# Optimization experiments

Measured on AMD Instinct MI355X. Metric: run time of the kernel, lower is better.

Reference implementation:

```python
import jax, jax.numpy as jnp
import numpy as np

N = 100000      # points
M = 12500       # cluster centers
E0 = 1600000    # point-level edges
E1 = 400000     # cluster-level edges
F_IN = 4        # raw point feature dim (e.g. intensity + extras)
D = 64          # hidden feature width
N_CLASSES = 8


def setup_inputs() -> dict:
    key = jax.random.key(0)
    ks = jax.random.split(key, 20)
    s = 0.05
    d = {}
    d["features"] = jax.random.normal(ks[0], (N, F_IN), jnp.float32)
    d["points"] = jax.random.normal(ks[1], (N, 3), jnp.float32)
    d["cluster_centers"] = jax.random.normal(ks[2], (M, 3), jnp.float32)
    d["l0_edges"] = jax.random.randint(ks[3], (E0, 2), 0, N)
    d["l1_edges"] = jax.random.randint(ks[4], (E1, 2), 0, M)
    d["labels"] = jax.random.randint(ks[5], (N,), 0, M)
    # Feature_extract MLP
    d["W_fe"] = s * jax.random.normal(ks[6], (F_IN + 3, D), jnp.float32)
    d["b_fe"] = jnp.zeros((D,), jnp.float32)
    # 4 Mini_GNN layers (layer2, layer2_1, layer6, layer6_1), stacked
    d["mini_We"] = s * jax.random.normal(ks[7], (4, D + 3, D), jnp.float32)
    d["mini_be"] = jnp.zeros((4, D), jnp.float32)
    d["mini_Wu"] = s * jax.random.normal(ks[8], (4, D, D), jnp.float32)
    d["mini_bu"] = jnp.zeros((4, D), jnp.float32)
    # Mini_to_Large
    d["W_m1"] = s * jax.random.normal(ks[9], (D + 3, D), jnp.float32)
    d["b_m1"] = jnp.zeros((D,), jnp.float32)
    d["W_m2"] = s * jax.random.normal(ks[10], (D, D), jnp.float32)
    d["b_m2"] = jnp.zeros((D,), jnp.float32)
    # 2 GNN layers on cluster graph (layer4, layer4_1), stacked
    d["gnn_We"] = s * jax.random.normal(ks[11], (2, D + 3, D), jnp.float32)
    d["gnn_be"] = jnp.zeros((2, D), jnp.float32)
    d["gnn_Wu"] = s * jax.random.normal(ks[12], (2, D, D), jnp.float32)
    d["gnn_bu"] = jnp.zeros((2, D), jnp.float32)
    # Large_to_Mini
    d["W_l"] = s * jax.random.normal(ks[13], (D + 3, D), jnp.float32)
    d["b_l"] = jnp.zeros((D,), jnp.float32)
    # Classifier
    d["W_c"] = s * jax.random.normal(ks[14], (D, N_CLASSES), jnp.float32)
    d["b_c"] = jnp.zeros((N_CLASSES,), jnp.float32)
    return d


def _gnn_layer(feat, pos, edges, We, be, Wu, bu, n_nodes):
    """PointGNN-style layer: gather -> edge MLP -> scatter max -> update MLP -> residual."""
    src, dst = edges[:, 0], edges[:, 1]
    e_in = jnp.concatenate([pos[src] - pos[dst], feat[src]], axis=-1)  # [E, 3+D]
    h = jax.nn.relu(e_in @ We + be)                                     # [E, D]
    agg = jax.ops.segment_max(h, dst, num_segments=n_nodes)            # [n, D]
    agg = jnp.where(jnp.isneginf(agg), 0.0, agg)  # nodes with no in-edges -> 0
    return jax.nn.relu(agg @ Wu + bu) + feat


def reference(features, points, cluster_centers, l0_edges, l1_edges, labels,
              W_fe, b_fe, mini_We, mini_be, mini_Wu, mini_bu,
              W_m1, b_m1, W_m2, b_m2, gnn_We, gnn_be, gnn_Wu, gnn_bu,
              W_l, b_l, W_c, b_c):
    rel = points - cluster_centers[labels]  # [N, 3] point pos relative to its cluster
    # layer1: Feature_extract
    f1 = jax.nn.relu(jnp.concatenate([features, rel], -1) @ W_fe + b_fe)
    # layer2 / layer2_1: Mini_GNN (scatter max) on point graph
    f2 = _gnn_layer(f1, points, l0_edges, mini_We[0], mini_be[0], mini_Wu[0], mini_bu[0], N)
    f2_1 = _gnn_layer(f2, points, l0_edges, mini_We[1], mini_be[1], mini_Wu[1], mini_bu[1], N)
    # layer3: Mini_to_Large (scatter sum by labels)
    h = jax.nn.relu(jnp.concatenate([f2_1, rel], -1) @ W_m1 + b_m1)
    c = jax.ops.segment_sum(h, labels, num_segments=M)  # [M, D]
    f3 = jax.nn.relu(c @ W_m2 + b_m2)
    # layer4 / layer4_1: GNN (scatter max) on cluster graph
    f4 = _gnn_layer(f3, cluster_centers, l1_edges, gnn_We[0], gnn_be[0], gnn_Wu[0], gnn_bu[0], M)
    f4_1 = _gnn_layer(f4, cluster_centers, l1_edges, gnn_We[1], gnn_be[1], gnn_Wu[1], gnn_bu[1], M)
    # layer5: Large_to_Mini (gather by labels)
    f5 = jax.nn.relu(jnp.concatenate([f4_1[labels], rel], -1) @ W_l + b_l)
    # layer6 / layer6_1 with residual skips per call()
    f6 = _gnn_layer(f5, points, l0_edges, mini_We[2], mini_be[2], mini_Wu[2], mini_bu[2], N)
    f6 = f6 + f2_1
    f6_1 = _gnn_layer(f6, points, l0_edges, mini_We[3], mini_be[3], mini_Wu[3], mini_bu[3], N)
    final = f6_1 + f2
    return final @ W_c + b_c  # [N, N_CLASSES] per-point logits
```

## Files before the change

### kernel.cpp

```cpp
#include <hip/hip_runtime.h>


#define N_PTS   100000
#define M_CL    12500
#define E0_N    1600000
#define E1_N    400000

#define NB      256
#define NCOPY   32
#define RANGE0  391
#define RANGE1  49
#define NCH0    782
#define NCH1    196
#define NCHL    49
#define CAP0    7168
#define CAP1    2048
#define CAPL    768

#define LSTR    72

typedef unsigned short ushortT;
typedef short  short8 __attribute__((ext_vector_type(8)));
typedef short  s4v    __attribute__((ext_vector_type(4)));
typedef float  v4f    __attribute__((ext_vector_type(4)));
typedef _Float16 h2   __attribute__((ext_vector_type(2)));
typedef unsigned u4v  __attribute__((ext_vector_type(4)));

__device__ inline ushortT f2bf(float x){
  union{float f; unsigned u;} v; v.f = x;
  unsigned r = v.u + 0x7fffu + ((v.u >> 16) & 1u);
  return (ushortT)(r >> 16);
}
__device__ inline float bf2f(ushortT h){
  union{unsigned u; float f;} v; v.u = ((unsigned)h) << 16;
  return v.f;
}
__device__ inline ushortT f2h(float x){
  union{_Float16 h; ushortT u;} v; v.h = (_Float16)x;
  return v.u;
}
__device__ inline float h2f(ushortT u){
  union{ushortT u; _Float16 h;} v; v.u = u;
  return (float)v.h;
}
__device__ inline h2 pkmax(h2 a, h2 b){ return __builtin_elementwise_max(a, b); }
__device__ inline h2 u2h(unsigned u){ union{unsigned u; h2 h;} v{u}; return v.h; }

struct WSrc { const float* p[22]; };


template<int RANGE, bool LAB>
__device__ void sort_chunk(const int* __restrict__ edges, int E, int c,
                           unsigned* __restrict__ slab, int* __restrict__ offC,
                           int* __restrict__ btot,
                           unsigned* slds, int* hist, int* pfx){
  int tid = threadIdx.x;
  int base = c*2048;
  int cnt = E - base; if (cnt > 2048) cnt = 2048;
  hist[tid] = 0;
  __syncthreads();
  int bk[8]; unsigned pk[8];
  #pragma unroll
  for (int r=0;r<8;++r){
    int e = base + r*256 + tid;
    bk[r] = -1; pk[r] = 0;
    if (e < E){
      int s, d;
      if (LAB){ s = e; d = edges[e]; }
      else    { int2 ed = ((const int2*)edges)[e]; s = ed.x; d = ed.y; }
      int b = d / RANGE;
      bk[r] = b;
      pk[r] = ((unsigned)s << 11) | (unsigned)(d - b*RANGE);
      atomicAdd(&hist[b], 1);
    }
  }
  __syncthreads();
  int own = hist[tid];
  pfx[tid] = own;
  __syncthreads();
  for (int st=1; st<256; st<<=1){
    int x = (tid >= st) ? pfx[tid-st] : 0;
    __syncthreads();
    pfx[tid] += x;
    __syncthreads();
  }
  int excl = pfx[tid] - own;
  offC[(size_t)c*257 + tid] = excl;
  if (tid == 0) offC[(size_t)c*257 + 256] = cnt;
  if (own) atomicAdd(&btot[(c & (NCOPY-1))*NB + tid], own);
  hist[tid] = excl;
  __syncthreads();
  #pragma unroll
  for (int r=0;r<8;++r){
    if (bk[r] >= 0){
      int pos = atomicAdd(&hist[bk[r]], 1);
      slds[pos] = pk[r];
    }
  }
  __syncthreads();
  unsigned* sg = slab + (size_t)c*2048;
  for (int i=tid; i<cnt; i+=256) sg[i] = slds[i];
}


template<int RANGE, int NCHUNK, int K>
__device__ void csr_build_seg(const unsigned* __restrict__ slab, const int* __restrict__ offC,
                              const int* __restrict__ btot,
                              int n, int* __restrict__ offs, int* __restrict__ csr,
                              int b, unsigned* stage, int* hist, int* part,
                              ushortT* mstA, ushortT* mlenA, ushortT* sbA){
  constexpr int CPT = (NCHUNK + 255) / 256;
  int tid = threadIdx.x;
  int dlo = b*RANGE;
  int range = n - dlo; if (range > RANGE) range = RANGE; if (range < 0) range = 0;
  int ownT = 0;
  #pragma unroll
  for (int k=0;k<NCOPY;++k) ownT += btot[k*NB + tid];
  part[tid] = ownT;
  __syncthreads();
  for (int st=1; st<256; st<<=1){
    int x = (tid >= st) ? part[tid-st] : 0;
    __syncthreads();
    part[tid] += x;
    __syncthreads();
  }
  int totB = part[b];
  int total = part[NB-1];
  if (b == NB-1 && tid == 0) offs[n] = total;
  __syncthreads();
  int mst[CPT], mlen[CPT];
  int csum = 0;
  #pragma unroll
  for (int k=0;k<CPT;++k){
    int c = tid + k*256;
    int l = 0, s0 = 0;
    if (c < NCHUNK){
      s0 = offC[(size_t)c*257 + b];
      l  = offC[(size_t)c*257 + b + 1] - s0;
    }
    mst[k] = s0; mlen[k] = l; csum += l;
  }
  part[tid] = csum;
  __syncthreads();
  int own2 = csum;
  for (int st=1; st<256; st<<=1){
    int x = (tid >= st) ? part[tid-st] : 0;
    __syncthreads();
    part[tid] += x;
    __syncthreads();
  }
  int cnt = part[NB-1];
  int gb = totB - cnt;
  int sb = part[tid] - own2;
  #pragma unroll
  for (int k=0;k<CPT;++k){
    int c = tid + k*256;
    if (c < NCHUNK){
      mstA[c] = (ushortT)mst[k];
      mlenA[c] = (ushortT)mlen[k];
      sbA[c] = (ushortT)sb;
      sb += mlen[k];
    }
  }
  __syncthreads();
  int wv = tid >> 6, l = tid & 63;
  for (int cb = wv*32; cb < NCHUNK; cb += 128){
    int c = cb + (l >> 1);
    if (c < NCHUNK){
      int len = mlenA[c];
      int half = l & 1;
      if (half*4 < len){
        const unsigned* sg = slab + (size_t)c*2048 + mstA[c];
        int sbc = sbA[c];
        for (int j = half*4; j < len; j += 8){
          unsigned v[4];
          __builtin_memcpy(v, sg + j, 16);
          #pragma unroll
          for (int q=0;q<4;++q) if (j+q < len) stage[sbc+j+q] = v[q];
        }
      }
    }
  }
  __syncthreads();
  for (int t=tid; t<RANGE; t+=256) hist[t] = 0;
  __syncthreads();
  for (int j=tid; j<cnt; j+=256) atomicAdd(&hist[stage[j] & 2047u], 1);
  __syncthreads();
  int s = 0; int loc[K];
  #pragma unroll
  for (int kk=0; kk<K; ++kk){
    int idx = tid*K + kk;
    int v = (idx < RANGE) ? hist[idx] : 0;
    loc[kk] = s; s += v;
  }
  part[tid] = s; __syncthreads();
  int own3 = s;
  for (int st=1; st<256; st<<=1){
    int x = (tid >= st) ? part[tid-st] : 0;
    __syncthreads();
    part[tid] += x;
    __syncthreads();
  }
  int ebase = part[tid] - own3;
  __syncthreads();
  #pragma unroll
  for (int kk=0; kk<K; ++kk){
    int idx = tid*K + kk;
    if (idx < RANGE){
      int ex = ebase + loc[kk];
      if (idx < range) offs[dlo+idx] = gb + ex;
      hist[idx] = ex;
    }
  }
  __syncthreads();
  for (int j=tid; j<cnt; j+=256){
    unsigned p = stage[j];
    int pos = atomicAdd(&hist[p & 2047u], 1);
    csr[gb + pos] = (int)(p >> 11);
  }
}

__global__ __launch_bounds__(256) void k_build_all(
    const unsigned* s0, const int* oc0, const int* bt0, int* offs0, int* csr0,
    const unsigned* s1, const int* oc1, const int* bt1, int* offs1, int* csr1,
    const unsigned* sL, const int* ocL, const int* btL, int* offsL, int* csrL){
  __shared__ unsigned stage[CAP0];
  __shared__ int hist[RANGE0];
  __shared__ int part[256];
  __shared__ ushortT mstA[NCH0];
  __shared__ ushortT mlenA[NCH0];
  __shared__ ushortT sbA[NCH0];
  int b = blockIdx.x;
  if (b < 256)      csr_build_seg<RANGE0,NCH0,2>(s0, oc0, bt0, N_PTS, offs0, csr0, b, stage, hist, part, mstA, mlenA, sbA);
  else if (b < 512) csr_build_seg<RANGE1,NCH1,1>(s1, oc1, bt1, M_CL, offs1, csr1, b-256, stage, hist, part, mstA, mlenA, sbA);
  else              csr_build_seg<RANGE1,NCHL,1>(sL, ocL, btL, M_CL, offsL, csrL, b-512, stage, hist, part, mstA, mlenA, sbA);
}


__global__ __launch_bounds__(256) void k_bin_f1g(
    WSrc s, ushortT* __restrict__ wt, ushortT* __restrict__ wtc, float* __restrict__ wpp,
    const int* __restrict__ l0e, const int* __restrict__ l1e, const int* __restrict__ labels,
    int* bt0, int* bt1, int* btL,
    unsigned* sl0, unsigned* sl1, unsigned* slL,
    int* oc0, int* oc1, int* ocL,
    const float* __restrict__ features, const float* __restrict__ points,
    const float* __restrict__ centers,
    const float* __restrict__ W, const float* __restrict__ bfe,
    const float* __restrict__ bias2, const float* __restrict__ We,
    float* __restrict__ rel, ushortT* __restrict__ f1b,
    ushortT* __restrict__ gout, int n, int ntiles, int nf1blk)
{
  __shared__ char smem[10240];
  int b = blockIdx.x;
  if (b < 17){
    int slot = b;
    if (slot < 15){
      const float* src = s.p[slot];
      ushortT* dst = wt + slot*4096;
      for (int e=threadIdx.x; e<4096; e+=256){
        int nn = e>>6, p = e&63;
        int kk = (p&3)*16 + (p>>2);
        dst[e] = f2bf(src[kk*64+nn]);
      }
    } else if (slot == 15){
      const float* src = s.p[15];
      for (int e=threadIdx.x; e<1024; e+=256){
        int nn = e>>6, p = e&63;
        int kk = (p&3)*16 + (p>>2);
        wtc[e] = (nn<8) ? f2bf(src[kk*8+nn]) : (ushortT)0;
      }
    } else {
      for (int e=threadIdx.x; e<6*192; e+=256){
        int i = e/192, rem = e - i*192, r = rem>>6, p = rem&63;
        wpp[e] = s.p[16+i][r*64 + ((p&3)*16 + (p>>2))];
      }
    }
    return;
  }
  b -= 17;
  if (b < 1027){
    unsigned* slds = (unsigned*)smem;
    int* hist = (int*)(smem + 8192);
    int* pfx  = (int*)(smem + 9216);
    if (b < 782)      sort_chunk<RANGE0,false>(l0e, E0_N, b,     sl0, oc0, bt0, slds, hist, pfx);
    else if (b < 978) sort_chunk<RANGE1,false>(l1e, E1_N, b-782, sl1, oc1, bt1, slds, hist, pfx);
    else              sort_chunk<RANGE1,true >(labels, N_PTS, b-978, slL, ocL, btL, slds, hist, pfx);
    return;
  }
  ushortT* lds = (ushortT*)smem;
  int bb = b - 1027;
  int tid = threadIdx.x;
  int lane = tid & 63, wslot = tid >> 6;
  int quad = lane >> 4, l15 = lane & 15;
  int permL = (lane & 15)*4 + (lane >> 4);
  int r3 = lane/3, c3 = lane - r3*3;
  int gw = (bb*256 + tid) >> 6;
  int nw = (nf1blk*256) >> 6;
  float Wf0=W[0*64+lane], Wf1=W[1*64+lane], Wf2=W[2*64+lane], Wf3=W[3*64+lane];
  float wr0=W[4*64+lane], wr1=W[5*64+lane], wr2=W[6*64+lane];
  float bias=bfe[lane];
  const float* Wk = We + 192;
  auto ldf = [&](int nn, int pbase)->short8{
    short8 r;
    #pragma unroll
    for (int e=0;e<8;++e){
      int p = pbase + e;
      int kk = (p&3)*16 + (p>>2);
      r[e] = (short)f2bf(Wk[kk*64 + nn]);
    }
    return r;
  };
  short8 s0_0 = ldf(l15, quad*8),      s0_1 = ldf(l15, 32+quad*8);
  short8 s1_0 = ldf(16+l15, quad*8),   s1_1 = ldf(16+l15, 32+quad*8);
  short8 s2_0 = ldf(32+l15, quad*8),   s2_1 = ldf(32+l15, 32+quad*8);
  short8 s3_0 = ldf(48+l15, quad*8),   s3_1 = ldf(48+l15, 32+quad*8);
  float eb0 = bias2[l15], eb1 = bias2[16+l15], eb2 = bias2[32+l15], eb3 = bias2[48+l15];
  float e0c0=We[0*64+l15], e0c1=We[0*64+16+l15], e0c2=We[0*64+32+l15], e0c3=We[0*64+48+l15];
  float e1c0=We[1*64+l15], e1c1=We[1*64+16+l15], e1c2=We[1*64+32+l15], e1c3=We[1*64+48+l15];
  float e2c0=We[2*64+l15], e2c1=We[2*64+16+l15], e2c2=We[2*64+32+l15], e2c3=We[2*64+48+l15];

  for (int t=gw; t<ntiles; t+=nw){
    int i0 = t*16;
    int lab16 = labels[min(i0 + (lane & 15), n-1)];
    float fv  = features[(size_t)min(i0 + (lane>>2), n-1)*4 + (lane & 3)];
    int lb = __shfl(lab16, (r3 < 16) ? r3 : 0, 64);
    float pv = 0.f, relv = 0.f;
    if (lane < 48){
      int rowp = i0 + r3;
      int rc = (rowp < n) ? rowp : (n-1);
      pv = points[(size_t)rc*3 + c3];
      float cv = centers[(size_t)lb*3 + c3];
      relv = pv - cv;
      if (rowp < n) rel[(size_t)rowp*3 + c3] = relv;
    }
    #pragma unroll
    for (int r=0;r<16;++r){
      float rx = __shfl(relv, 3*r+0, 64);
      float ry = __shfl(relv, 3*r+1, 64);
      float rz = __shfl(relv, 3*r+2, 64);
      float f0 = __shfl(fv, 4*r+0, 64);
      float f1 = __shfl(fv, 4*r+1, 64);
      float f2 = __shfl(fv, 4*r+2, 64);
      float f3 = __shfl(fv, 4*r+3, 64);
      float acc = bias + wr0*rx + wr1*ry + wr2*rz;
      acc += f0*Wf0 + f1*Wf1;
      acc += f2*Wf2 + f3*Wf3;
      acc = fmaxf(acc, 0.f);
      ushortT ab = f2bf(acc);
      int row = i0 + r;
      if (row < n) f1b[(size_t)row*64 + permL] = ab;
      lds[wslot*(16*LSTR) + r*LSTR + permL] = ab;
    }
    __builtin_amdgcn_wave_barrier();
    const ushortT* lp = lds + wslot*(16*LSTR) + l15*LSTR + quad*8;
    short8 sa0 = *(const short8*)(lp);
    short8 sa1 = *(const short8*)(lp + 32);
    __builtin_amdgcn_wave_barrier();
    v4f ec0 = {0.f,0.f,0.f,0.f}, ec1 = ec0, ec2 = ec0, ec3 = ec0;
    ec0 = __builtin_amdgcn_mfma_f32_16x16x32_bf16(sa0, s0_0, ec0, 0,0,0);
    ec1 = __builtin_amdgcn_mfma_f32_16x16x32_bf16(sa0, s1_0, ec1, 0,0,0);
    ec2 = __builtin_amdgcn_mfma_f32_16x16x32_bf16(sa0, s2_0, ec2, 0,0,0);
    ec3 = __builtin_amdgcn_mfma_f32_16x16x32_bf16(sa0, s3_0, ec3, 0,0,0);
    ec0 = __builtin_amdgcn_mfma_f32_16x16x32_bf16(sa1, s0_1, ec0, 0,0,0);
    ec1 = __builtin_amdgcn_mfma_f32_16x16x32_bf16(sa1, s1_1, ec1, 0,0,0);
    ec2 = __builtin_amdgcn_mfma_f32_16x16x32_bf16(sa1, s2_1, ec2, 0,0,0);
    ec3 = __builtin_amdgcn_mfma_f32_16x16x32_bf16(sa1, s3_1, ec3, 0,0,0);
    #pragma unroll
    for (int r=0;r<4;++r){
      int row = i0 + quad*4 + r;
      if (row < n){
        int rr4 = quad*4 + r;
        float vx = __shfl(pv, 3*rr4+0, 64);
        float vy = __shfl(pv, 3*rr4+1, 64);
        float vz = __shfl(pv, 3*rr4+2, 64);
        float g0 = ec0[r] + eb0 + vx*e0c0 + vy*e1c0 + vz*e2c0;
        float g1 = ec1[r] + eb1 + vx*e0c1 + vy*e1c1 + vz*e2c1;
        float g2 = ec2[r] + eb2 + vx*e0c2 + vy*e1c2 + vz*e2c2;
        float g3 = ec3[r] + eb3 + vx*e0c3 + vy*e1c3 + vz*e2c3;
        s4v o; o.x=(short)f2h(g0); o.y=(short)f2h(g1); o.z=(short)f2h(g2); o.w=(short)f2h(g3);
        *(s4v*)(gout + (size_t)row*64 + l15*4) = o;
      }
    }
  }
}


template<bool RELU, int NRES, bool USEREL, bool GATHER, bool OUT16, bool F16O, int EMODE, bool ERELU>
__global__ __launch_bounds__(256) void k_gemm(
    const ushortT* __restrict__ A, const ushortT* __restrict__ Wt,
    const float* __restrict__ bias, const float* __restrict__ Wr,
    const float* __restrict__ rel, const int* __restrict__ gidx,
    const ushortT* __restrict__ r1, const ushortT* __restrict__ r2,
    ushortT* __restrict__ out16,
    const ushortT* __restrict__ Wt2, const float* __restrict__ bias2,
    const float* __restrict__ Wr2, const float* __restrict__ vec2,
    void* __restrict__ eout,
    int n, int ntiles)
{
  constexpr int LDSZ = (EMODE>0) ? 4*16*LSTR : 4;
  __shared__ ushortT lds[LDSZ];
  int tid = threadIdx.x;
  int lane = tid & 63, wslot = tid >> 6;
  int quad = lane >> 4, l15 = lane & 15;
  int r3 = lane/3, c3 = lane - r3*3;
  int gw = (blockIdx.x*256 + tid) >> 6;
  int nw = (gridDim.x*256) >> 6;

  short8 bfr0_0 = *(const short8*)(Wt + ( 0 + l15)*64 +  0 + quad*8);
  short8 bfr0_1 = *(const short8*)(Wt + ( 0 + l15)*64 + 32 + quad*8);
  short8 bfr1_0 = *(const short8*)(Wt + (16 + l15)*64 +  0 + quad*8);
  short8 bfr1_1 = *(const short8*)(Wt + (16 + l15)*64 + 32 + quad*8);
  short8 bfr2_0 = *(const short8*)(Wt + (32 + l15)*64 +  0 + quad*8);
  short8 bfr2_1 = *(const short8*)(Wt + (32 + l15)*64 + 32 + quad*8);
  short8 bfr3_0 = *(const short8*)(Wt + (48 + l15)*64 +  0 + quad*8);
  short8 bfr3_1 = *(const short8*)(Wt + (48 + l15)*64 + 32 + quad*8);
  float bs0 = bias[ 0 + l15], bs1 = bias[16 + l15];
  float bs2 = bias[32 + l15], bs3 = bias[48 + l15];
  float w0c0=0,w0c1=0,w0c2=0,w0c3=0, w1c0=0,w1c1=0,w1c2=0,w1c3=0, w2c0=0,w2c1=0,w2c2=0,w2c3=0;
  if (USEREL){
    w0c0=Wr[0*64+l15]; w0c1=Wr[0*64+16+l15]; w0c2=Wr[0*64+32+l15]; w0c3=Wr[0*64+48+l15];
    w1c0=Wr[1*64+l15]; w1c1=Wr[1*64+16+l15]; w1c2=Wr[1*64+32+l15]; w1c3=Wr[1*64+48+l15];
    w2c0=Wr[2*64+l15]; w2c1=Wr[2*64+16+l15]; w2c2=Wr[2*64+32+l15]; w2c3=Wr[2*64+48+l15];
  }

  short8 s0_0{}, s0_1{}, s1_0{}, s1_1{}, s2_0{}, s2_1{}, s3_0{}, s3_1{};
  float eb0=0, eb1=0, eb2=0, eb3=0;
  float e0c0=0,e0c1=0,e0c2=0,e0c3=0, e1c0=0,e1c1=0,e1c2=0,e1c3=0, e2c0=0,e2c1=0,e2c2=0,e2c3=0;
  float ebias_c = 0.f;
  if (EMODE == 1){
    s0_0 = *(const short8*)(Wt2 + ( 0 + l15)*64 +  0 + quad*8);
    s0_1 = *(const short8*)(Wt2 + ( 0 + l15)*64 + 32 + quad*8);
    s1_0 = *(const short8*)(Wt2 + (16 + l15)*64 +  0 + quad*8);
    s1_1 = *(const short8*)(Wt2 + (16 + l15)*64 + 32 + quad*8);
    s2_0 = *(const short8*)(Wt2 + (32 + l15)*64 +  0 + quad*8);
    s2_1 = *(const short8*)(Wt2 + (32 + l15)*64 + 32 + quad*8);
    s3_0 = *(const short8*)(Wt2 + (48 + l15)*64 +  0 + quad*8);
    s3_1 = *(const short8*)(Wt2 + (48 + l15)*64 + 32 + quad*8);
    eb0 = bias2[l15]; eb1 = bias2[16+l15]; eb2 = bias2[32+l15]; eb3 = bias2[48+l15];
    e0c0=Wr2[0*64+l15]; e0c1=Wr2[0*64+16+l15]; e0c2=Wr2[0*64+32+l15]; e0c3=Wr2[0*64+48+l15];
    e1c0=Wr2[1*64+l15]; e1c1=Wr2[1*64+16+l15]; e1c2=Wr2[1*64+32+l15]; e1c3=Wr2[1*64+48+l15];
    e2c0=Wr2[2*64+l15]; e2c1=Wr2[2*64+16+l15]; e2c2=Wr2[2*64+32+l15]; e2c3=Wr2[2*64+48+l15];
  } else if (EMODE == 2){
    s0_0 = *(const short8*)(Wt2 + l15*64 +  0 + quad*8);
    s0_1 = *(const short8*)(Wt2 + l15*64 + 32 + quad*8);
    ebias_c = (l15 < 8) ? bias2[l15] : 0.f;
  }

  for (int t=gw; t<ntiles; t+=nw){
    int i0 = t*16;
    int rowA = i0 + l15; if (rowA >= n) rowA = n-1;
    if (GATHER) rowA = gidx[rowA];
    const ushortT* ap = A + (size_t)rowA*64 + quad*8;
    short8 a0 = *(const short8*)(ap);
    short8 a1 = *(const short8*)(ap + 32);
    float relL = 0.f;
    if (USEREL && lane < 48){
      int rc = i0 + r3; if (rc >= n) rc = n-1;
      relL = rel[(size_t)rc*3 + c3];
    }
    v4f ac0 = {0.f,0.f,0.f,0.f}, ac1 = ac0, ac2 = ac0, ac3 = ac0;
    ac0 = __builtin_amdgcn_mfma_f32_16x16x32_bf16(a0, bfr0_0, ac0, 0,0,0);
    ac1 = __builtin_amdgcn_mfma_f32_16x16x32_bf16(a0, bfr1_0, ac1, 0,0,0);
    ac2 = __builtin_amdgcn_mfma_f32_16x16x32_bf16(a0, bfr2_0, ac2, 0,0,0);
    ac3 = __builtin_amdgcn_mfma_f32_16x16x32_bf16(a0, bfr3_0, ac3, 0,0,0);
    ac0 = __builtin_amdgcn_mfma_f32_16x16x32_bf16(a1, bfr0_1, ac0, 0,0,0);
    ac1 = __builtin_amdgcn_mfma_f32_16x16x32_bf16(a1, bfr1_1, ac1, 0,0,0);
    ac2 = __builtin_amdgcn_mfma_f32_16x16x32_bf16(a1, bfr2_1, ac2, 0,0,0);
    ac3 = __builtin_amdgcn_mfma_f32_16x16x32_bf16(a1, bfr3_1, ac3, 0,0,0);

    #pragma unroll
    for (int r=0;r<4;++r){
      int row = i0 + quad*4 + r;
      bool rowok = (row < n);
      float v0 = ac0[r] + bs0, v1 = ac1[r] + bs1, v2 = ac2[r] + bs2, v3 = ac3[r] + bs3;
      if (USEREL){
        int rr4 = quad*4 + r;
        float rx = __shfl(relL, 3*rr4+0, 64);
        float ry = __shfl(relL, 3*rr4+1, 64);
        float rz = __shfl(relL, 3*rr4+2, 64);
        v0 += rx*w0c0 + ry*w1c0 + rz*w2c0;
        v1 += rx*w0c1 + ry*w1c1 + rz*w2c1;
        v2 += rx*w0c2 + ry*w1c2 + rz*w2c2;
        v3 += rx*w0c3 + ry*w1c3 + rz*w2c3;
      }
      if (RELU){ v0=fmaxf(v0,0.f); v1=fmaxf(v1,0.f); v2=fmaxf(v2,0.f); v3=fmaxf(v3,0.f); }
      size_t pb = (size_t)row*64 + l15*4;
      if (rowok){
        if (NRES>=1){
          s4v rv = *(const s4v*)(r1 + pb);
          v0 += bf2f((ushortT)rv.x); v1 += bf2f((ushortT)rv.y);
          v2 += bf2f((ushortT)rv.z); v3 += bf2f((ushortT)rv.w);
        }
        if (NRES>=2){
          s4v rv = *(const s4v*)(r2 + pb);
          v0 += bf2f((ushortT)rv.x); v1 += bf2f((ushortT)rv.y);
          v2 += bf2f((ushortT)rv.z); v3 += bf2f((ushortT)rv.w);
        }
        if (OUT16){
          s4v o;
          if (F16O){ o.x=(short)f2h(v0); o.y=(short)f2h(v1); o.z=(short)f2h(v2); o.w=(short)f2h(v3); }
          else     { o.x=(short)f2bf(v0); o.y=(short)f2bf(v1); o.z=(short)f2bf(v2); o.w=(short)f2bf(v3); }
          *(s4v*)(out16 + pb) = o;
        }
      }
      if (EMODE > 0){
        int lb = wslot*(16*LSTR) + (quad*4+r)*LSTR + l15*4;
        s4v o; o.x=(short)f2bf(v0); o.y=(short)f2bf(v1); o.z=(short)f2bf(v2); o.w=(short)f2bf(v3);
        *(s4v*)(lds + lb) = o;
      }
    }

    if (EMODE > 0){
      __builtin_amdgcn_wave_barrier();
      const ushortT* lp = lds + wslot*(16*LSTR) + l15*LSTR + quad*8;
      short8 sa0 = *(const short8*)(lp);
      short8 sa1 = *(const short8*)(lp + 32);
      __builtin_amdgcn_wave_barrier();
      if (EMODE == 1){
        float posv = 0.f;
        if (lane < 48){
          int rc = i0 + r3; if (rc >= n) rc = n-1;
          posv = vec2[(size_t)rc*3 + c3];
        }
        v4f ec0 = {0.f,0.f,0.f,0.f}, ec1 = ec0, ec2 = ec0, ec3 = ec0;
        ec0 = __builtin_amdgcn_mfma_f32_16x16x32_bf16(sa0, s0_0, ec0, 0,0,0);
        ec1 = __builtin_amdgcn_mfma_f32_16x16x32_bf16(sa0, s1_0, ec1, 0,0,0);
        ec2 = __builtin_amdgcn_mfma_f32_16x16x32_bf16(sa0, s2_0, ec2, 0,0,0);
        ec3 = __builtin_amdgcn_mfma_f32_16x16x32_bf16(sa0, s3_0, ec3, 0,0,0);
        ec0 = __builtin_amdgcn_mfma_f32_16x16x32_bf16(sa1, s0_1, ec0, 0,0,0);
        ec1 = __builtin_amdgcn_mfma_f32_16x16x32_bf16(sa1, s1_1, ec1, 0,0,0);
        ec2 = __builtin_amdgcn_mfma_f32_16x16x32_bf16(sa1, s2_1, ec2, 0,0,0);
        ec3 = __builtin_amdgcn_mfma_f32_16x16x32_bf16(sa1, s3_1, ec3, 0,0,0);
        ushortT* eo = (ushortT*)eout;
        #pragma unroll
        for (int r=0;r<4;++r){
          int row = i0 + quad*4 + r;
          if (row < n){
            int rr4 = quad*4 + r;
            float vx = __shfl(posv, 3*rr4+0, 64);
            float vy = __shfl(posv, 3*rr4+1, 64);
            float vz = __shfl(posv, 3*rr4+2, 64);
            float g0 = ec0[r] + eb0 + vx*e0c0 + vy*e1c0 + vz*e2c0;
            float g1 = ec1[r] + eb1 + vx*e0c1 + vy*e1c1 + vz*e2c1;
            float g2 = ec2[r] + eb2 + vx*e0c2 + vy*e1c2 + vz*e2c2;
            float g3 = ec3[r] + eb3 + vx*e0c3 + vy*e1c3 + vz*e2c3;
            if (ERELU){ g0=fmaxf(g0,0.f); g1=fmaxf(g1,0.f); g2=fmaxf(g2,0.f); g3=fmaxf(g3,0.f); }
            s4v o; o.x=(short)f2h(g0); o.y=(short)f2h(g1); o.z=(short)f2h(g2); o.w=(short)f2h(g3);
            *(s4v*)(eo + (size_t)row*64 + l15*4) = o;
          }
        }
      } else {
        v4f ec = {0.f,0.f,0.f,0.f};
        ec = __builtin_amdgcn_mfma_f32_16x16x32_bf16(sa0, s0_0, ec, 0,0,0);
        ec = __builtin_amdgcn_mfma_f32_16x16x32_bf16(sa1, s0_1, ec, 0,0,0);
        if (l15 < 8){
          float* eo = (float*)eout;
          #pragma unroll
          for (int r=0;r<4;++r){
            int row = i0 + quad*4 + r;
            if (row < n) eo[(size_t)row*8 + l15] = ec[r] + ebias_c;
          }
        }
      }
    }
  }
}


__global__ __launch_bounds__(256) void k_edge_agg(const int* __restrict__ offs, const int* __restrict__ csr,
                                                  const float* __restrict__ pos, const ushortT* __restrict__ g,
                                                  const float* __restrict__ Wp, ushortT* __restrict__ agg, int n){
  int lane = threadIdx.x & 63;
  int grp = lane >> 3, d8 = lane & 7;
  int gbase = lane & 56;
  int gw = (blockIdx.x*256 + threadIdx.x) >> 6;
  int nw = (gridDim.x*256) >> 6;
  const u4v* g4 = (const u4v*)g;
  float2 w0[4], w1[4], w2[4];
  #pragma unroll
  for (int q=0;q<4;++q){
    w0[q] = *(const float2*)(Wp + 0*64 + d8*8 + 2*q);
    w1[q] = *(const float2*)(Wp + 1*64 + d8*8 + 2*q);
    w2[q] = *(const float2*)(Wp + 2*64 + d8*8 + 2*q);
  }
  const h2 NEGBIG = {(_Float16)-60000.f, (_Float16)-60000.f};
  int n8 = (n+7) >> 3;
  for (int ii=gw; ii<n8; ii+=nw){
    int i0 = ii*8;
    int ig = i0 + grp; bool ok = ig < n; if (!ok) ig = n-1;
    int b = offs[ig], e = offs[ig+1];
    int cnt = e - b, c1 = cnt - 1;
    int mx = cnt;
    mx = max(mx, __shfl_xor(mx, 8, 64));
    mx = max(mx, __shfl_xor(mx, 16, 64));
    mx = max(mx, __shfl_xor(mx, 32, 64));
    h2 m0=NEGBIG, m1=NEGBIG, m2=NEGBIG, m3=NEGBIG;
    for (int J=0; J<mx; J+=8){
      if (J < cnt){
        int sv = csr[b + min(J + d8, c1)];
        #pragma unroll
        for (int jj=0; jj<8; ++jj){
          int s = __shfl(sv, gbase + jj, 64);
          u4v u = g4[(size_t)s*8 + d8];
          m0 = pkmax(m0, u2h(u.x));
          m1 = pkmax(m1, u2h(u.y));
          m2 = pkmax(m2, u2h(u.z));
          m3 = pkmax(m3, u2h(u.w));
        }
      }
    }
    float px = pos[ig*3+0], py = pos[ig*3+1], pz = pos[ig*3+2];
    u4v outv;
    {
      float sA = w0[0].x*px + w1[0].x*py + w2[0].x*pz;
      float sB = w0[0].y*px + w1[0].y*py + w2[0].y*pz;
      outv.x = (unsigned)f2bf(fmaxf((float)m0.x - sA, 0.f)) |
               ((unsigned)f2bf(fmaxf((float)m0.y - sB, 0.f)) << 16);
    }
    {
      float sA = w0[1].x*px + w1[1].x*py + w2[1].x*pz;
      float sB = w0[1].y*px + w1[1].y*py + w2[1].y*pz;
      outv.y = (unsigned)f2bf(fmaxf((float)m1.x - sA, 0.f)) |
               ((unsigned)f2bf(fmaxf((float)m1.y - sB, 0.f)) << 16);
    }
    {
      float sA = w0[2].x*px + w1[2].x*py + w2[2].x*pz;
      float sB = w0[2].y*px + w1[2].y*py + w2[2].y*pz;
      outv.z = (unsigned)f2bf(fmaxf((float)m2.x - sA, 0.f)) |
               ((unsigned)f2bf(fmaxf((float)m2.y - sB, 0.f)) << 16);
    }
    {
      float sA = w0[3].x*px + w1[3].x*py + w2[3].x*pz;
      float sB = w0[3].y*px + w1[3].y*py + w2[3].y*pz;
      outv.w = (unsigned)f2bf(fmaxf((float)m3.x - sA, 0.f)) |
               ((unsigned)f2bf(fmaxf((float)m3.y - sB, 0.f)) << 16);
    }
    if (ok) ((u4v*)agg)[(size_t)ig*8 + d8] = outv;
  }
}


__global__ __launch_bounds__(256) void k_seg_gather(const int* __restrict__ offs, const int* __restrict__ csr,
                                                    const ushortT* __restrict__ h, ushortT* __restrict__ c, int m){
  int lane = threadIdx.x & 63;
  int wv = (blockIdx.x*256 + threadIdx.x) >> 6;
  if (wv >= m) return;
  int b = offs[wv], e = offs[wv+1];
  float acc = 0.f;
  for (int k=b; k<e; ++k){
    int i = csr[k];
    acc += h2f(h[(size_t)i*64+lane]);
  }
  c[(size_t)wv*64+lane] = f2bf(acc);
}


extern "C" void kernel_launch(void* const* d_in, const int* in_sizes, int n_in,
                              void* d_out, int out_size, void* d_ws, size_t ws_size,
                              hipStream_t stream){
  const float* features = (const float*)d_in[0];
  const float* points   = (const float*)d_in[1];
  const float* centers  = (const float*)d_in[2];
  const int*   l0e      = (const int*)d_in[3];
  const int*   l1e      = (const int*)d_in[4];
  const int*   labels   = (const int*)d_in[5];
  const float* W_fe = (const float*)d_in[6];
  const float* b_fe = (const float*)d_in[7];
  const float* mWe  = (const float*)d_in[8];
  const float* mbe  = (const float*)d_in[9];
  const float* mWu  = (const float*)d_in[10];
  const float* mbu  = (const float*)d_in[11];
  const float* W_m1 = (const float*)d_in[12];
  const float* b_m1 = (const float*)d_in[13];
  const float* W_m2 = (const float*)d_in[14];
  const float* b_m2 = (const float*)d_in[15];
  const float* gWe  = (const float*)d_in[16];
  const float* gbe  = (const float*)d_in[17];
  const float* gWu  = (const float*)d_in[18];
  const float* gbu  = (const float*)d_in[19];
  const float* W_l  = (const float*)d_in[20];
  const float* b_l  = (const float*)d_in[21];
  const float* W_c  = (const float*)d_in[22];
  const float* b_c  = (const float*)d_in[23];
  float* out = (float*)d_out;

  char* w = (char*)d_ws;
  size_t off = 0;
  auto alloc = [&](size_t bytes)->void*{
    void* p = (void*)(w + off);
    off = (off + bytes + 255) & ~(size_t)255;
    return p;
  };
  float* rel  = (float*)alloc((size_t)N_PTS*3*4);
  ushortT* UF1 = (ushortT*)alloc((size_t)N_PTS*64*2);
  ushortT* UF2 = (ushortT*)alloc((size_t)N_PTS*64*2);
  ushortT* UF21= (ushortT*)alloc((size_t)N_PTS*64*2);
  ushortT* UF5 = (ushortT*)alloc((size_t)N_PTS*64*2);
  ushortT* UF6 = (ushortT*)alloc((size_t)N_PTS*64*2);
  ushortT* gbuf= (ushortT*)alloc((size_t)N_PTS*64*2);
  ushortT* abuf= (ushortT*)alloc((size_t)N_PTS*64*2);
  ushortT* cb_b= (ushortT*)alloc((size_t)M_CL*64*2);
  ushortT* UF3 = (ushortT*)alloc((size_t)M_CL*64*2);
  ushortT* UF4 = (ushortT*)alloc((size_t)M_CL*64*2);
  ushortT* cg_b= (ushortT*)alloc((size_t)M_CL*64*2);
  ushortT* cagg_b = (ushortT*)alloc((size_t)M_CL*64*2);
  ushortT* f41_b  = (ushortT*)alloc((size_t)M_CL*64*2);
  ushortT* wt  = (ushortT*)alloc((size_t)15*4096*2);
  ushortT* wtc = (ushortT*)alloc((size_t)1024*2);
  float* wpp = (float*)alloc((size_t)6*192*4);
  int* offs0 = (int*)alloc((size_t)(N_PTS+1)*4);
  int* csr0  = (int*)alloc((size_t)E0_N*4);
  int* offs1 = (int*)alloc((size_t)(M_CL+1)*4);
  int* csr1  = (int*)alloc((size_t)E1_N*4);
  int* offsL = (int*)alloc((size_t)(M_CL+1)*4);
  int* csrL  = (int*)alloc((size_t)N_PTS*4);
  unsigned* slab0 = (unsigned*)alloc((size_t)NCH0*2048*4);
  unsigned* slab1 = (unsigned*)alloc((size_t)NCH1*2048*4);
  unsigned* slabL = (unsigned*)alloc((size_t)NCHL*2048*4);
  int* offC0 = (int*)alloc((size_t)NCH0*257*4);
  int* offC1 = (int*)alloc((size_t)NCH1*257*4);
  int* offCL = (int*)alloc((size_t)NCHL*257*4);
  int* btotA = (int*)alloc((size_t)3*NCOPY*NB*4);
  int* btot0 = btotA;
  int* btot1 = btotA + NCOPY*NB;
  int* btotL = btotA + 2*NCOPY*NB;
  (void)ws_size; (void)in_sizes; (void)n_in; (void)out_size;

  const int NT_N = (N_PTS+15)/16;
  const int NT_M = (M_CL +15)/16;
  const int GBG_N = 1563;
  const int GBG_M = 196;
  const int GB_N  = 3125;
  const int GB_BIN = 17 + 1027;

  WSrc ws{};
  ws.p[0]=mWu+0*4096; ws.p[1]=mWu+1*4096; ws.p[2]=mWu+2*4096; ws.p[3]=mWu+3*4096;
  ws.p[4]=W_m2; ws.p[5]=gWu+0*4096; ws.p[6]=gWu+1*4096;
  ws.p[7]=mWe+0*4288+192; ws.p[8]=mWe+1*4288+192; ws.p[9]=mWe+2*4288+192; ws.p[10]=mWe+3*4288+192;
  ws.p[11]=W_m1; ws.p[12]=W_l; ws.p[13]=gWe+0*4288+192; ws.p[14]=gWe+1*4288+192;
  ws.p[15]=W_c;
  ws.p[16]=mWe+0*4288; ws.p[17]=mWe+1*4288; ws.p[18]=mWe+2*4288; ws.p[19]=mWe+3*4288;
  ws.p[20]=gWe+0*4288; ws.p[21]=gWe+1*4288;

  hipMemsetAsync(btotA, 0, (size_t)3*NCOPY*NB*4, stream);
  k_bin_f1g<<<GB_BIN + GBG_N, 256, 0, stream>>>(ws, wt, wtc, wpp,
      l0e, l1e, labels, btot0, btot1, btotL,
      slab0, slab1, slabL, offC0, offC1, offCL,
      features, points, centers, W_fe, b_fe, mbe, mWe,
      rel, UF1, gbuf, N_PTS, NT_N, GBG_N);
  k_build_all<<<768, 256, 0, stream>>>(slab0, offC0, btot0, offs0, csr0,
                                       slab1, offC1, btot1, offs1, csr1,
                                       slabL, offCL, btotL, offsL, csrL);

  k_edge_agg<<<GB_N,256,0,stream>>>(offs0, csr0, points, gbuf, wpp+0*192, abuf, N_PTS);
  k_gemm<true,1,false,false,true,false,1,false><<<GBG_N,256,0,stream>>>(abuf, wt+0*4096, mbu+0,
      nullptr, nullptr, nullptr, UF1, nullptr, UF2,
      wt+8*4096, mbe+64, mWe+1*4288, points, gbuf, N_PTS, NT_N);
  k_edge_agg<<<GB_N,256,0,stream>>>(offs0, csr0, points, gbuf, wpp+1*192, abuf, N_PTS);
  k_gemm<true,1,false,false,true,false,1,true><<<GBG_N,256,0,stream>>>(abuf, wt+1*4096, mbu+64,
      nullptr, nullptr, nullptr, UF2, nullptr, UF21,
      wt+11*4096, b_m1, W_m1+4096, rel, gbuf, N_PTS, NT_N);
  k_seg_gather<<<(M_CL*64+255)/256, 256, 0, stream>>>(offsL, csrL, gbuf, cb_b, M_CL);
  k_gemm<true,0,false,false,true,false,1,false><<<GBG_M,256,0,stream>>>(cb_b, wt+4*4096, b_m2,
      nullptr, nullptr, nullptr, nullptr, nullptr, UF3,
      wt+13*4096, gbe+0, gWe+0*4288, centers, cg_b, M_CL, NT_M);
  k_edge_agg<<<GBG_M,256,0,stream>>>(offs1, csr1, centers, cg_b, wpp+4*192, cagg_b, M_CL);
  k_gemm<true,1,false,false,true,false,1,false><<<GBG_M,256,0,stream>>>(cagg_b, wt+5*4096, gbu+0,
      nullptr, nullptr, nullptr, UF3, nullptr, UF4,
      wt+14*4096, gbe+64, gWe+1*4288, centers, cg_b, M_CL, NT_M);
  k_edge_agg<<<GBG_M,256,0,stream>>>(offs1, csr1, centers, cg_b, wpp+5*192, cagg_b, M_CL);
  k_gemm<true,1,false,false,true,false,0,false><<<GBG_M,256,0,stream>>>(cagg_b, wt+6*4096, gbu+64,
      nullptr, nullptr, nullptr, UF4, nullptr, f41_b,
      nullptr, nullptr, nullptr, nullptr, nullptr, M_CL, NT_M);
  k_gemm<true,0,true,true,true,false,1,false><<<GBG_N,256,0,stream>>>(f41_b, wt+12*4096, b_l,
      W_l+4096, rel, labels, nullptr, nullptr, UF5,
      wt+9*4096, mbe+128, mWe+2*4288, points, gbuf, N_PTS, NT_N);
  k_edge_agg<<<GB_N,256,0,stream>>>(offs0, csr0, points, gbuf, wpp+2*192, abuf, N_PTS);
  k_gemm<true,2,false,false,true,false,1,false><<<GBG_N,256,0,stream>>>(abuf, wt+2*4096, mbu+128,
      nullptr, nullptr, nullptr, UF5, UF21, UF6,
      wt+10*4096, mbe+192, mWe+3*4288, points, gbuf, N_PTS, NT_N);
  k_edge_agg<<<GB_N,256,0,stream>>>(offs0, csr0, points, gbuf, wpp+3*192, abuf, N_PTS);
  k_gemm<true,2,false,false,false,false,2,false><<<GBG_N,256,0,stream>>>(abuf, wt+3*4096, mbu+192,
      nullptr, nullptr, nullptr, UF6, UF2, nullptr,
      wtc, b_c, nullptr, nullptr, out, N_PTS, NT_N);
}
```

Measured before the change: 450.1 us.

## Fuse cluster-level GNN chain into one persistent kernel with grid barriers

```diff
diff --git a/kernel.cpp b/kernel.cpp
--- a/kernel.cpp
+++ b/kernel.cpp
@@ -14,8 +14,6 @@
 #define NCH1    196
 #define NCHL    49
 #define CAP0    7168
-#define CAP1    2048
-#define CAPL    768
 
 #define LSTR    72
 
@@ -47,6 +45,18 @@
 __device__ inline h2 u2h(unsigned u){ union{unsigned u; h2 h;} v{u}; return v.h; }
 
 struct WSrc { const float* p[22]; };
+
+
+__device__ inline void gridbar(int* bar, int nblk){
+  __syncthreads();
+  if (threadIdx.x == 0){
+    __threadfence();
+    atomicAdd(bar, 1);
+    while (atomicAdd(bar, 0) < nblk) {}
+    __threadfence();
+  }
+  __syncthreads();
+}
 
 
 template<int RANGE, bool LAB>
@@ -386,7 +396,7 @@
 
 
 template<bool RELU, int NRES, bool USEREL, bool GATHER, bool OUT16, bool F16O, int EMODE, bool ERELU>
-__global__ __launch_bounds__(256) void k_gemm(
+__device__ void gemm_body(
     const ushortT* __restrict__ A, const ushortT* __restrict__ Wt,
     const float* __restrict__ bias, const float* __restrict__ Wr,
     const float* __restrict__ rel, const int* __restrict__ gidx,
@@ -395,16 +405,12 @@
     const ushortT* __restrict__ Wt2, const float* __restrict__ bias2,
     const float* __restrict__ Wr2, const float* __restrict__ vec2,
     void* __restrict__ eout,
-    int n, int ntiles)
+    int n, int ntiles, int gw, int nw, ushortT* lds)
 {
-  constexpr int LDSZ = (EMODE>0) ? 4*16*LSTR : 4;
-  __shared__ ushortT lds[LDSZ];
   int tid = threadIdx.x;
   int lane = tid & 63, wslot = tid >> 6;
   int quad = lane >> 4, l15 = lane & 15;
   int r3 = lane/3, c3 = lane - r3*3;
-  int gw = (blockIdx.x*256 + tid) >> 6;
-  int nw = (gridDim.x*256) >> 6;
 
   short8 bfr0_0 = *(const short8*)(Wt + ( 0 + l15)*64 +  0 + quad*8);
   short8 bfr0_1 = *(const short8*)(Wt + ( 0 + l15)*64 + 32 + quad*8);
@@ -566,15 +572,35 @@
   }
 }
 
-
-__global__ __launch_bounds__(256) void k_edge_agg(const int* __restrict__ offs, const int* __restrict__ csr,
-                                                  const float* __restrict__ pos, const ushortT* __restrict__ g,
-                                                  const float* __restrict__ Wp, ushortT* __restrict__ agg, int n){
+template<bool RELU, int NRES, bool USEREL, bool GATHER, bool OUT16, bool F16O, int EMODE, bool ERELU>
+__global__ __launch_bounds__(256) void k_gemm(
+    const ushortT* __restrict__ A, const ushortT* __restrict__ Wt,
+    const float* __restrict__ bias, const float* __restrict__ Wr,
+    const float* __restrict__ rel, const int* __restrict__ gidx,
+    const ushortT* __restrict__ r1, const ushortT* __restrict__ r2,
+    ushortT* __restrict__ out16,
+    const ushortT* __restrict__ Wt2, const float* __restrict__ bias2,
+    const float* __restrict__ Wr2, const float* __restrict__ vec2,
+    void* __restrict__ eout,
+    int n, int ntiles)
+{
+  constexpr int LDSZ = (EMODE>0) ? 4*16*LSTR : 4;
+  __shared__ ushortT lds[LDSZ];
+  int gw = (blockIdx.x*256 + threadIdx.x) >> 6;
+  int nw = (gridDim.x*256) >> 6;
+  gemm_body<RELU,NRES,USEREL,GATHER,OUT16,F16O,EMODE,ERELU>(
+      A, Wt, bias, Wr, rel, gidx, r1, r2, out16, Wt2, bias2, Wr2, vec2, eout,
+      n, ntiles, gw, nw, lds);
+}
+
+
+__device__ void agg_body(const int* __restrict__ offs, const int* __restrict__ csr,
+                         const float* __restrict__ pos, const ushortT* __restrict__ g,
+                         const float* __restrict__ Wp, ushortT* __restrict__ agg, int n,
+                         int gw, int nw){
   int lane = threadIdx.x & 63;
   int grp = lane >> 3, d8 = lane & 7;
   int gbase = lane & 56;
-  int gw = (blockIdx.x*256 + threadIdx.x) >> 6;
-  int nw = (gridDim.x*256) >> 6;
   const u4v* g4 = (const u4v*)g;
   float2 w0[4], w1[4], w2[4];
   #pragma unroll
@@ -639,19 +665,66 @@
   }
 }
 
-
-__global__ __launch_bounds__(256) void k_seg_gather(const int* __restrict__ offs, const int* __restrict__ csr,
-                                                    const ushortT* __restrict__ h, ushortT* __restrict__ c, int m){
+__global__ __launch_bounds__(256) void k_edge_agg(const int* __restrict__ offs, const int* __restrict__ csr,
+                                                  const float* __restrict__ pos, const ushortT* __restrict__ g,
+                                                  const float* __restrict__ Wp, ushortT* __restrict__ agg, int n){
+  int gw = (blockIdx.x*256 + threadIdx.x) >> 6;
+  int nw = (gridDim.x*256) >> 6;
+  agg_body(offs, csr, pos, g, Wp, agg, n, gw, nw);
+}
+
+
+__device__ void seg_body(const int* __restrict__ offs, const int* __restrict__ csr,
+                         const ushortT* __restrict__ h, ushortT* __restrict__ c, int m,
+                         int wv0, int nwv){
   int lane = threadIdx.x & 63;
-  int wv = (blockIdx.x*256 + threadIdx.x) >> 6;
-  if (wv >= m) return;
-  int b = offs[wv], e = offs[wv+1];
-  float acc = 0.f;
-  for (int k=b; k<e; ++k){
-    int i = csr[k];
-    acc += h2f(h[(size_t)i*64+lane]);
-  }
-  c[(size_t)wv*64+lane] = f2bf(acc);
+  for (int wv = wv0; wv < m; wv += nwv){
+    int b = offs[wv], e = offs[wv+1];
+    float acc = 0.f;
+    for (int k=b; k<e; ++k){
+      int i = csr[k];
+      acc += h2f(h[(size_t)i*64+lane]);
+    }
+    c[(size_t)wv*64+lane] = f2bf(acc);
+  }
+}
+
+
+#define MCH_BLK 256
+
+__global__ __launch_bounds__(256) void k_mchain(
+    const int* __restrict__ offsL, const int* __restrict__ csrL,
+    const ushortT* __restrict__ gbuf, ushortT* __restrict__ cb_b,
+    const ushortT* __restrict__ wt, const float* __restrict__ b_m2,
+    const float* __restrict__ gbe, const float* __restrict__ gbu,
+    const float* __restrict__ gWe, const float* __restrict__ centers,
+    const int* __restrict__ offs1, const int* __restrict__ csr1,
+    const float* __restrict__ wpp,
+    ushortT* __restrict__ cg_b, ushortT* __restrict__ cagg_b,
+    ushortT* __restrict__ UF3, ushortT* __restrict__ UF4, ushortT* __restrict__ f41_b,
+    int* __restrict__ bar, int ntM)
+{
+  __shared__ ushortT lds[4*16*LSTR];
+  int gw = (blockIdx.x*256 + threadIdx.x) >> 6;
+  int nw = (MCH_BLK*256) >> 6;
+
+  seg_body(offsL, csrL, gbuf, cb_b, M_CL, gw, nw);
+  gridbar(bar+0, MCH_BLK);
+  gemm_body<true,0,false,false,true,false,1,false>(cb_b, wt+4*4096, b_m2,
+      nullptr, nullptr, nullptr, nullptr, nullptr, UF3,
+      wt+13*4096, gbe+0, gWe+0*4288, centers, cg_b, M_CL, ntM, gw, nw, lds);
+  gridbar(bar+1, MCH_BLK);
+  agg_body(offs1, csr1, centers, cg_b, wpp+4*192, cagg_b, M_CL, gw, nw);
+  gridbar(bar+2, MCH_BLK);
+  gemm_body<true,1,false,false,true,false,1,false>(cagg_b, wt+5*4096, gbu+0,
+      nullptr, nullptr, nullptr, UF3, nullptr, UF4,
+      wt+14*4096, gbe+64, gWe+1*4288, centers, cg_b, M_CL, ntM, gw, nw, lds);
+  gridbar(bar+3, MCH_BLK);
+  agg_body(offs1, csr1, centers, cg_b, wpp+5*192, cagg_b, M_CL, gw, nw);
+  gridbar(bar+4, MCH_BLK);
+  gemm_body<true,1,false,false,true,false,0,false>(cagg_b, wt+6*4096, gbu+64,
+      nullptr, nullptr, nullptr, UF4, nullptr, f41_b,
+      nullptr, nullptr, nullptr, nullptr, nullptr, M_CL, ntM, gw, nw, lds);
 }
 
 
@@ -720,16 +793,16 @@
   int* offC0 = (int*)alloc((size_t)NCH0*257*4);
   int* offC1 = (int*)alloc((size_t)NCH1*257*4);
   int* offCL = (int*)alloc((size_t)NCHL*257*4);
-  int* btotA = (int*)alloc((size_t)3*NCOPY*NB*4);
+  int* btotA = (int*)alloc((size_t)(3*NCOPY*NB + 64)*4);
   int* btot0 = btotA;
   int* btot1 = btotA + NCOPY*NB;
   int* btotL = btotA + 2*NCOPY*NB;
+  int* bar   = btotA + 3*NCOPY*NB;
   (void)ws_size; (void)in_sizes; (void)n_in; (void)out_size;
 
   const int NT_N = (N_PTS+15)/16;
   const int NT_M = (M_CL +15)/16;
   const int GBG_N = 1563;
-  const int GBG_M = 196;
   const int GB_N  = 3125;
   const int GB_BIN = 17 + 1027;
 
@@ -742,7 +815,7 @@
   ws.p[16]=mWe+0*4288; ws.p[17]=mWe+1*4288; ws.p[18]=mWe+2*4288; ws.p[19]=mWe+3*4288;
   ws.p[20]=gWe+0*4288; ws.p[21]=gWe+1*4288;
 
-  hipMemsetAsync(btotA, 0, (size_t)3*NCOPY*NB*4, stream);
+  hipMemsetAsync(btotA, 0, (size_t)(3*NCOPY*NB + 64)*4, stream);
   k_bin_f1g<<<GB_BIN + GBG_N, 256, 0, stream>>>(ws, wt, wtc, wpp,
       l0e, l1e, labels, btot0, btot1, btotL,
       slab0, slab1, slabL, offC0, offC1, offCL,
@@ -760,18 +833,9 @@
   k_gemm<true,1,false,false,true,false,1,true><<<GBG_N,256,0,stream>>>(abuf, wt+1*4096, mbu+64,
       nullptr, nullptr, nullptr, UF2, nullptr, UF21,
       wt+11*4096, b_m1, W_m1+4096, rel, gbuf, N_PTS, NT_N);
-  k_seg_gather<<<(M_CL*64+255)/256, 256, 0, stream>>>(offsL, csrL, gbuf, cb_b, M_CL);
-  k_gemm<true,0,false,false,true,false,1,false><<<GBG_M,256,0,stream>>>(cb_b, wt+4*4096, b_m2,
-      nullptr, nullptr, nullptr, nullptr, nullptr, UF3,
-      wt+13*4096, gbe+0, gWe+0*4288, centers, cg_b, M_CL, NT_M);
-  k_edge_agg<<<GBG_M,256,0,stream>>>(offs1, csr1, centers, cg_b, wpp+4*192, cagg_b, M_CL);
-  k_gemm<true,1,false,false,true,false,1,false><<<GBG_M,256,0,stream>>>(cagg_b, wt+5*4096, gbu+0,
-      nullptr, nullptr, nullptr, UF3, nullptr, UF4,
-      wt+14*4096, gbe+64, gWe+1*4288, centers, cg_b, M_CL, NT_M);
-  k_edge_agg<<<GBG_M,256,0,stream>>>(offs1, csr1, centers, cg_b, wpp+5*192, cagg_b, M_CL);
-  k_gemm<true,1,false,false,true,false,0,false><<<GBG_M,256,0,stream>>>(cagg_b, wt+6*4096, gbu+64,
-      nullptr, nullptr, nullptr, UF4, nullptr, f41_b,
-      nullptr, nullptr, nullptr, nullptr, nullptr, M_CL, NT_M);
+  k_mchain<<<MCH_BLK,256,0,stream>>>(offsL, csrL, gbuf, cb_b,
+      wt, b_m2, gbe, gbu, gWe, centers,
+      offs1, csr1, wpp, cg_b, cagg_b, UF3, UF4, f41_b, bar, NT_M);
   k_gemm<true,0,true,true,true,false,1,false><<<GBG_N,256,0,stream>>>(f41_b, wt+12*4096, b_l,
       W_l+4096, rel, labels, nullptr, nullptr, UF5,
       wt+9*4096, mbe+128, mWe+2*4288, points, gbuf, N_PTS, NT_N);
```

Result: slower. 602.8 us (+33.9%).
